# Performance work log

Hardware: AMD Instinct MI355X
Metric: run time of the kernel (lower is better)

## Reference

```python
import jax, jax.numpy as jnp
import numpy as np
from jax import lax

EPS = 1e-5
# PyTorch bicubic (a=-0.75), scale_factor=2, align_corners=False -> fixed 4-tap
# weights: even outputs use frac 0.75, odd outputs use frac 0.25.
W75 = jnp.array([-0.03515625, 0.26171875, 0.87890625, -0.10546875], dtype=jnp.float32)
W25 = W75[::-1]


def _up1d_2x(x, axis):
    x = jnp.moveaxis(x, axis, -1)
    n = x.shape[-1]
    pad = [(0, 0)] * (x.ndim - 1) + [(2, 2)]
    xp = jnp.pad(x, pad, mode='edge')  # replicate border like torch
    even = sum(W75[k] * xp[..., k:k + n] for k in range(4))
    odd = sum(W25[k] * xp[..., k + 1:k + 1 + n] for k in range(4))
    out = jnp.stack([even, odd], axis=-1).reshape(x.shape[:-1] + (2 * n,))
    return jnp.moveaxis(out, -1, axis)


def bicubic2x(x):  # [N,C,H,W] -> [N,C,2H,2W]
    return _up1d_2x(_up1d_2x(x, 2), 3)


def groupnorm1(x, w, b):  # GroupNorm(1, C): normalize over (C,H,W) per sample
    m = jnp.mean(x, axis=(1, 2, 3), keepdims=True)
    v = jnp.mean(jnp.square(x - m), axis=(1, 2, 3), keepdims=True)
    xh = (x - m) * lax.rsqrt(v + EPS)
    return xh * w[None, :, None, None] + b[None, :, None, None]


def conv3x3(x, w, b):
    y = lax.conv_general_dilated(x, w, (1, 1), ((1, 1), (1, 1)),
                                 dimension_numbers=('NCHW', 'OIHW', 'NCHW'))
    return y + b[None, :, None, None]


def setup_inputs() -> dict:
    key = jax.random.key(0)
    ks = jax.random.split(key, 24)
    B, C, H, W = 4, 256, 64, 64
    chans = [256, 64, 16, 4]  # embed_dim // 4**i
    inp = {'x': jax.random.normal(ks[0], (B, C, H, W), jnp.float32)}
    for j in range(4):
        s = 2 ** (j + 1)
        inp[f'em{j}'] = 0.1 * jax.random.normal(ks[1 + j], (B, chans[j], H * s, W * s), jnp.float32)
    for j, c in enumerate(chans):
        co = max(c // 4, 1)
        inp[f'gn_w{j}'] = 1.0 + 0.1 * jax.random.normal(ks[5 + 4 * j], (c,), jnp.float32)
        inp[f'gn_b{j}'] = 0.1 * jax.random.normal(ks[6 + 4 * j], (c,), jnp.float32)
        inp[f'cw{j}'] = jax.random.normal(ks[7 + 4 * j], (co, c, 3, 3), jnp.float32) / np.sqrt(9.0 * c)
        inp[f'cb{j}'] = 0.01 * jax.random.normal(ks[8 + 4 * j], (co,), jnp.float32)
    # per-sample (left, top, right, bottom) in the 64x64 grid; host-side ints
    # (in the original these come from get_bbox_from_mask on CPU)
    inp['bboxes'] = np.array([[8, 4, 56, 60], [0, 0, 48, 40],
                              [16, 8, 64, 56], [4, 12, 40, 64]], dtype=np.int32)
    return inp


def reference(x, em0, em1, em2, em3,
              gn_w0, gn_b0, cw0, cb0, gn_w1, gn_b1, cw1, cb1,
              gn_w2, gn_b2, cw2, cb2, gn_w3, gn_b3, cw3, cb3, bboxes):
    ems = [em0, em1, em2, em3]
    gws = [gn_w0, gn_w1, gn_w2, gn_w3]
    gbs = [gn_b0, gn_b1, gn_b2, gn_b3]
    cws = [cw0, cw1, cw2, cw3]
    cbs = [cb0, cb1, cb2, cb3]
    bb = np.asarray(bboxes)
    strides = [2, 4, 8, 16]
    B, _, H, W = x.shape
    mask = jnp.full((B, 1, H * 16, W * 16), -100.0, dtype=x.dtype)
    for i in range(B):  # per-sample ragged regions, as in the original eval loop
        l, t, r, b = (int(v) for v in bb[i])
        z = x[i:i + 1, :, t:b, l:r]
        for j in range(4):
            z = groupnorm1(z, gws[j], gbs[j])
            z = bicubic2x(z)
            s = strides[j]
            z = z + ems[j][i:i + 1, :, t * s:b * s, l * s:r * s]
            z = conv3x3(z, cws[j], cbs[j])
            if j < 3:
                z = jax.nn.silu(z)
        s = strides[-1]
        mask = mask.at[i:i + 1, :, t * s:b * s, l * s:r * s].set(z)
    return mask
```

## Files before the change

### kernel.cpp

```cpp
#include <hip/hip_runtime.h>

#define EPS 1e-5f

__global__ void fill_kernel(float* __restrict__ out, int n, float v) {
    int i = blockIdx.x * blockDim.x + threadIdx.x;
    if (i < n) out[i] = v;
}

__global__ void zero8_kernel(float* __restrict__ a) {
    if (threadIdx.x < 8) a[threadIdx.x] = 0.f;
}

__global__ void finalize_kernel(float* __restrict__ buf, long long batchStride,
                                int n, int ocShift, const float* __restrict__ bias,
                                int doSilu)
{
    int idx = blockIdx.x * blockDim.x + threadIdx.x;
    if (idx >= n) return;
    float* p = buf + (long long)blockIdx.y * batchStride;
    int oc = idx >> ocShift;
    float v = p[idx] + bias[oc];
    if (doSilu) v = v / (1.f + __expf(-v));
    p[idx] = v;
}

__global__ void gn_reduce_kernel(const float* __restrict__ in, long long inBatchStride,
                                 int inPitch, long long inPlane, int useOrig,
                                 int c, int shift, const int* __restrict__ bboxes,
                                 int batch0, float* __restrict__ accs)
{
    int batch = batch0 + blockIdx.z;
    const int* bb = bboxes + 4 * batch;
    int l = bb[0], t = bb[1], r = bb[2], btm = bb[3];
    int h = (btm - t) << shift;
    int w = (r   - l) << shift;
    int oy = useOrig ? t : 0;
    int ox = useOrig ? l : 0;
    const float* base = in + (long long)blockIdx.z * inBatchStride;

    float s = 0.f, s2 = 0.f;
    int stride = gridDim.x * blockDim.x;

    if (((w | ox | inPitch) & 3) == 0) {
        int w4 = w >> 2;
        int count4 = c * h * w4;
        for (int idx = blockIdx.x * blockDim.x + threadIdx.x; idx < count4; idx += stride) {
            int xw   = idx % w4;
            int rest = idx / w4;
            int y    = rest % h;
            int ch   = rest / h;
            const float4 v = *reinterpret_cast<const float4*>(
                base + (long long)ch * inPlane + (long long)(y + oy) * inPitch + (ox + 4 * xw));
            s  += (v.x + v.y) + (v.z + v.w);
            s2 += (v.x * v.x + v.y * v.y) + (v.z * v.z + v.w * v.w);
        }
    } else {
        int count = c * h * w;
        for (int idx = blockIdx.x * blockDim.x + threadIdx.x; idx < count; idx += stride) {
            int xw   = idx % w;
            int rest = idx / w;
            int y    = rest % h;
            int ch   = rest / h;
            float v = base[(long long)ch * inPlane + (long long)(y + oy) * inPitch + (xw + ox)];
            s  += v;
            s2 += v * v;
        }
    }

    for (int off = 32; off > 0; off >>= 1) {
        s  += __shfl_down(s, off);
        s2 += __shfl_down(s2, off);
    }
    __shared__ float red[2][4];
    int wid = threadIdx.x >> 6;
    if ((threadIdx.x & 63) == 0) { red[0][wid] = s; red[1][wid] = s2; }
    __syncthreads();
    if (threadIdx.x == 0) {
        float ts = (red[0][0] + red[0][1]) + (red[0][2] + red[0][3]);
        float t2 = (red[1][0] + red[1][1]) + (red[1][2] + red[1][3]);
        atomicAdd(&accs[2 * batch],     ts);
        atomicAdd(&accs[2 * batch + 1], t2);
    }
}

__global__ void normup_kernel(const float* __restrict__ in, long long inBatchStride,
                              int inPitch, long long inPlane, int useOrig,
                              const float* __restrict__ em, long long emBatchStride, int emPitch,
                              const float* __restrict__ gw, const float* __restrict__ gb,
                              const float* __restrict__ accs,
                              float* __restrict__ outB, long long outBatchStride, int outPitch,
                              int c, int shift, const int* __restrict__ bboxes,
                              int batch0, int tilesY)
{
    int batch = batch0 + blockIdx.z;
    const int* bb = bboxes + 4 * batch;
    int l = bb[0], t = bb[1], r = bb[2], btm = bb[3];
    int h = (btm - t) << shift;
    int w = (r   - l) << shift;
    int H2 = 2 * h, W2 = 2 * w;

    int ch = blockIdx.y / tilesY;
    int ty = blockIdx.y % tilesY;
    int y2 = ty * 16 + threadIdx.y;
    int x2 = blockIdx.x * 16 + threadIdx.x;
    if (y2 >= H2 || x2 >= W2) return;

    float count = (float)(c * h * w);
    float m  = accs[2 * batch] / count;
    float var = accs[2 * batch + 1] / count - m * m;
    float rs = rsqrtf(fmaxf(var, 0.f) + EPS);
    float alpha = rs * gw[ch];
    float beta  = gb[ch] - m * alpha;

    int oy = useOrig ? t : 0;
    int ox = useOrig ? l : 0;
    const float* base = in + (long long)blockIdx.z * inBatchStride + (long long)ch * inPlane;

    const float Wv[2][4] = {
        {-0.03515625f, 0.26171875f, 0.87890625f, -0.10546875f},
        {-0.10546875f, 0.87890625f, 0.26171875f, -0.03515625f}};

    int iy = y2 >> 1, py = y2 & 1;
    int ix = x2 >> 1, px = x2 & 1;
    int by = iy - 2 + py;
    int bx = ix - 2 + px;

    float acc = 0.f;
    #pragma unroll
    for (int a = 0; a < 4; a++) {
        int ry = by + a;
        ry = ry < 0 ? 0 : (ry > h - 1 ? h - 1 : ry);
        const float* rowp = base + (long long)(ry + oy) * inPitch + ox;
        float rsum = 0.f;
        #pragma unroll
        for (int q = 0; q < 4; q++) {
            int rx = bx + q;
            rx = rx < 0 ? 0 : (rx > w - 1 ? w - 1 : rx);
            rsum += Wv[px][q] * rowp[rx];
        }
        acc += Wv[py][a] * rsum;
    }

    float val = alpha * acc + beta;
    int S = 2 << shift;
    val += em[(long long)blockIdx.z * emBatchStride + (long long)ch * emPitch * emPitch
              + (long long)(t * S + y2) * emPitch + (l * S + x2)];

    outB[(long long)blockIdx.z * outBatchStride + (long long)ch * outPitch * outPitch
         + (long long)y2 * outPitch + x2] = val;
}

#define CICH 4

template<int COT>
__global__ void __launch_bounds__(256)
conv_reg_kernel(const float* __restrict__ inB, long long inBatchStride, int inPitch,
                const float* __restrict__ wts, const float* __restrict__ bias,
                int cin, int ciPer, int bShift, int doSilu,
                float* __restrict__ out, long long outBatchStride, int outPitch,
                int toMask, int doFinal, int shift, const int* __restrict__ bboxes,
                int batch0, int tilesY)
{
    int zb = blockIdx.z & ((1 << bShift) - 1);
    int sp = blockIdx.z >> bShift;
    int batch = batch0 + zb;
    const int* bb = bboxes + 4 * batch;
    int l = bb[0], t = bb[1], r = bb[2], btm = bb[3];
    int h = (btm - t) << shift;
    int w = (r   - l) << shift;
    int H2 = 2 * h, W2 = 2 * w;

    int og = blockIdx.y / tilesY;
    int ty = blockIdx.y % tilesY;
    int oc0 = og * COT;
    int y0 = ty * 32;
    int x0 = blockIdx.x * 32;
    if (y0 >= H2 || x0 >= W2) return;

    int ly = threadIdx.y, lx = threadIdx.x;
    int tid = ly * 16 + lx;
    int py0 = y0 + 2 * ly;
    int px0 = x0 + 2 * lx;

    __shared__ float tile[CICH][34][36];
    __shared__ __align__(16) float wsh[COT][CICH][12];

    const float* base = inB + (long long)zb * inBatchStride;
    long long plane = (long long)inPitch * inPitch;
    long long oplane = (long long)outPitch * outPitch;

    constexpr int TITEMS = CICH * 1156;
    constexpr int NIT    = (TITEMS + 255) / 256;
    constexpr int WITEMS = COT * CICH * 9;
    constexpr int NWIT   = (WITEMS + 255) / 256;

    float acc[COT][2][2];
    #pragma unroll
    for (int o = 0; o < COT; o++)
        #pragma unroll
        for (int rr = 0; rr < 2; rr++)
            #pragma unroll
            for (int ss = 0; ss < 2; ss++) acc[o][rr][ss] = 0.f;

    int ciStart = sp * ciPer;
    int ciEnd = ciStart + ciPer;
    for (int ci0 = ciStart; ci0 < ciEnd; ci0 += CICH) {
        float rbuf[NIT];
        #pragma unroll
        for (int it = 0; it < NIT; ++it) {
            int q = tid + it * 256;
            float v = 0.f;
            if (q < TITEMS) {
                int p   = q / 1156;
                int rem = q - p * 1156;
                int yy  = rem / 34;
                int xx  = rem - yy * 34;
                int gy = y0 - 1 + yy, gx = x0 - 1 + xx;
                if (gy >= 0 && gy < H2 && gx >= 0 && gx < W2)
                    v = base[(long long)(ci0 + p) * plane + (long long)gy * inPitch + gx];
            }
            rbuf[it] = v;
        }
        float wreg[NWIT];
        #pragma unroll
        for (int it = 0; it < NWIT; ++it) {
            int q = tid + it * 256;
            float v = 0.f;
            if (q < WITEMS) {
                int o   = q / (CICH * 9);
                int rem = q - o * (CICH * 9);
                int p   = rem / 9;
                int k   = rem - p * 9;
                v = wts[((long long)(oc0 + o) * cin + (ci0 + p)) * 9 + k];
            }
            wreg[it] = v;
        }
        #pragma unroll
        for (int it = 0; it < NIT; ++it) {
            int q = tid + it * 256;
            if (q < TITEMS) {
                int p   = q / 1156;
                int rem = q - p * 1156;
                int yy  = rem / 34;
                int xx  = rem - yy * 34;
                tile[p][yy][xx] = rbuf[it];
            }
        }
        #pragma unroll
        for (int it = 0; it < NWIT; ++it) {
            int q = tid + it * 256;
            if (q < WITEMS) {
                int o   = q / (CICH * 9);
                int rem = q - o * (CICH * 9);
                int p   = rem / 9;
                int k   = rem - p * 9;
                wsh[o][p][k] = wreg[it];
            }
        }
        __syncthreads();

        #pragma unroll
        for (int p = 0; p < CICH; p++) {
            float v[4][4];
            #pragma unroll
            for (int rr = 0; rr < 4; rr++) {
                const float2 a = *reinterpret_cast<const float2*>(&tile[p][2 * ly + rr][2 * lx]);
                const float2 b = *reinterpret_cast<const float2*>(&tile[p][2 * ly + rr][2 * lx + 2]);
                v[rr][0] = a.x; v[rr][1] = a.y; v[rr][2] = b.x; v[rr][3] = b.y;
            }
            #pragma unroll
            for (int o = 0; o < COT; o++) {
                const float4 wA = *reinterpret_cast<const float4*>(&wsh[o][p][0]);
                const float4 wB = *reinterpret_cast<const float4*>(&wsh[o][p][4]);
                const float  w8 = wsh[o][p][8];
                #pragma unroll
                for (int rr = 0; rr < 2; rr++) {
                    #pragma unroll
                    for (int ss = 0; ss < 2; ss++) {
                        acc[o][rr][ss] += wA.x * v[rr    ][ss] + wA.y * v[rr    ][ss + 1] + wA.z * v[rr    ][ss + 2]
                                        + wA.w * v[rr + 1][ss] + wB.x * v[rr + 1][ss + 1] + wB.y * v[rr + 1][ss + 2]
                                        + wB.z * v[rr + 2][ss] + wB.w * v[rr + 2][ss + 1] + w8   * v[rr + 2][ss + 2];
                    }
                }
            }
        }
        __syncthreads();
    }

    if (doFinal) {
        #pragma unroll
        for (int o = 0; o < COT; o++) {
            float b = bias[oc0 + o];
            #pragma unroll
            for (int rr = 0; rr < 2; rr++) {
                #pragma unroll
                for (int ss = 0; ss < 2; ss++) {
                    int oy2 = py0 + rr, ox2 = px0 + ss;
                    if (oy2 >= H2 || ox2 >= W2) continue;
                    float v = acc[o][rr][ss] + b;
                    if (doSilu) v = v / (1.f + __expf(-v));
                    if (toMask) {
                        int S = 2 << shift;
                        out[(long long)batch * 1024 * 1024 + (long long)(t * S + oy2) * 1024 + (l * S + ox2)] = v;
                    } else {
                        out[(long long)zb * outBatchStride + (long long)(oc0 + o) * oplane
                            + (long long)oy2 * outPitch + ox2] = v;
                    }
                }
            }
        }
    } else {
        #pragma unroll
        for (int o = 0; o < COT; o++) {
            #pragma unroll
            for (int rr = 0; rr < 2; rr++) {
                #pragma unroll
                for (int ss = 0; ss < 2; ss++) {
                    int oy2 = py0 + rr, ox2 = px0 + ss;
                    if (oy2 >= H2 || ox2 >= W2) continue;
                    atomicAdd(&out[(long long)zb * outBatchStride + (long long)(oc0 + o) * oplane
                                   + (long long)oy2 * outPitch + ox2], acc[o][rr][ss]);
                }
            }
        }
    }
}

static inline void launch_conv(int co, int tiles32, int nz, int S,
                               const float* inB, long long inBS, int inPitch,
                               const float* wts, const float* bias, int cin, int doSilu,
                               float* out, long long outBS, int outPitch,
                               int toMask, int shift, const int* bboxes, int batch0,
                               hipStream_t stream)
{
    dim3 blk(16, 16);
    int bShift = (nz == 4) ? 2 : 0;
    int ciPer = cin / S;
    int doFinal = (S == 1) ? 1 : 0;
    dim3 grid;
    if (co == 64)      grid = dim3(tiles32, tiles32 * 8, nz * S);
    else if (co == 16) grid = dim3(tiles32, tiles32 * 2, nz * S);
    else               grid = dim3(tiles32, tiles32,     nz * S);

    if (co == 64 || co == 16) {
        conv_reg_kernel<8><<<grid, blk, 0, stream>>>(
            inB, inBS, inPitch, wts, bias, cin, ciPer, bShift, doSilu,
            out, outBS, outPitch, toMask, doFinal, shift, bboxes, batch0, tiles32);
    } else if (co == 4) {
        conv_reg_kernel<4><<<grid, blk, 0, stream>>>(
            inB, inBS, inPitch, wts, bias, cin, ciPer, bShift, doSilu,
            out, outBS, outPitch, toMask, doFinal, shift, bboxes, batch0, tiles32);
    } else {
        conv_reg_kernel<1><<<grid, blk, 0, stream>>>(
            inB, inBS, inPitch, wts, bias, cin, ciPer, bShift, doSilu,
            out, outBS, outPitch, toMask, doFinal, shift, bboxes, batch0, tiles32);
    }
}

extern "C" void kernel_launch(void* const* d_in, const int* in_sizes, int n_in,
                              void* d_out, int out_size, void* d_ws, size_t ws_size,
                              hipStream_t stream)
{
    const float* x  = (const float*)d_in[0];
    const float* em[4];
    const float* gw[4];
    const float* gb[4];
    const float* cw[4];
    const float* cb[4];
    for (int j = 0; j < 4; j++) {
        em[j] = (const float*)d_in[1 + j];
        gw[j] = (const float*)d_in[5 + 4 * j];
        gb[j] = (const float*)d_in[6 + 4 * j];
        cw[j] = (const float*)d_in[7 + 4 * j];
        cb[j] = (const float*)d_in[8 + 4 * j];
    }
    const int* bboxes = (const int*)d_in[21];
    float* out = (float*)d_out;
    float* ws  = (float*)d_ws;

    const int chans[4] = {256, 64, 16, 4};
    const int couts[4] = {64, 16, 4, 1};
    const int splits[4] = {1, 1, 1, 1};

    const long long A_OFF  = 256;
    const long long A_SLOT = 1048576;
    const long long B_SLOT = 4194304;

    bool par = ws_size >= (size_t)(A_OFF + 4 * A_SLOT + 4 * B_SLOT) * 4;
    int nA = par ? 4 : 1;
    float* accs = ws;
    float* bufA = ws + A_OFF;
    float* bufB = ws + A_OFF + nA * A_SLOT;

    fill_kernel<<<(4194304 + 255) / 256, 256, 0, stream>>>(out, 4194304, -100.0f);

    if (par) {
        for (int j = 0; j < 4; j++) {
            int c = chans[j], co = couts[j], shift = j;
            int inPitch = 64 << j;
            long long inPlane = (long long)inPitch * inPitch;
            int upPitch = 128 << j;
            int tiles = upPitch / 16;
            int tiles32 = upPitch / 32;
            int E = 128 << j;
            long long emStride = (long long)c * E * E;
            int S = splits[j];

            const float* gin = (j == 0) ? x : bufA;
            long long ginStride = (j == 0) ? (long long)256 * 64 * 64 : A_SLOT;
            int useOrig = (j == 0) ? 1 : 0;

            zero8_kernel<<<1, 64, 0, stream>>>(accs);
            gn_reduce_kernel<<<dim3(512, 1, 4), 256, 0, stream>>>(
                gin, ginStride, inPitch, inPlane, useOrig, c, shift, bboxes, 0, accs);
            normup_kernel<<<dim3(tiles, tiles * c, 4), dim3(16, 16), 0, stream>>>(
                gin, ginStride, inPitch, inPlane, useOrig,
                em[j], emStride, E, gw[j], gb[j], accs,
                bufB, B_SLOT, upPitch, c, shift, bboxes, 0, tiles);
            if (S > 1) {
                fill_kernel<<<(int)((4 * A_SLOT + 255) / 256), 256, 0, stream>>>(
                    bufA, (int)(4 * A_SLOT), 0.f);
            }
            launch_conv(co, tiles32, 4, S,
                        bufB, B_SLOT, upPitch, cw[j], cb[j], c, (j < 3) ? 1 : 0,
                        (j < 3) ? bufA : out, (j < 3) ? A_SLOT : 0, upPitch,
                        (j == 3) ? 1 : 0, shift, bboxes, 0, stream);
            if (S > 1) {
                int ocShift = 2 * (7 + j);
                finalize_kernel<<<dim3(4096, 4), 256, 0, stream>>>(
                    bufA, A_SLOT, (int)A_SLOT, ocShift, cb[j], (j < 3) ? 1 : 0);
            }
        }
    } else {
        for (int i = 0; i < 4; i++) {
            for (int j = 0; j < 4; j++) {
                int c = chans[j], co = couts[j], shift = j;
                int inPitch = 64 << j;
                long long inPlane = (long long)inPitch * inPitch;
                int upPitch = 128 << j;
                int tiles = upPitch / 16;
                int tiles32 = upPitch / 32;
                int E = 128 << j;
                long long emStride = (long long)c * E * E;
                int S = splits[j];

                const float* gin = (j == 0) ? (x + (long long)i * 256 * 64 * 64) : bufA;
                int useOrig = (j == 0) ? 1 : 0;

                zero8_kernel<<<1, 64, 0, stream>>>(accs);
                gn_reduce_kernel<<<dim3(512, 1, 1), 256, 0, stream>>>(
                    gin, 0, inPitch, inPlane, useOrig, c, shift, bboxes, i, accs);
                normup_kernel<<<dim3(tiles, tiles * c, 1), dim3(16, 16), 0, stream>>>(
                    gin, 0, inPitch, inPlane, useOrig,
                    em[j] + (long long)i * emStride, 0, E, gw[j], gb[j], accs,
                    bufB, 0, upPitch, c, shift, bboxes, i, tiles);
                if (S > 1) {
                    fill_kernel<<<(int)((A_SLOT + 255) / 256), 256, 0, stream>>>(
                        bufA, (int)A_SLOT, 0.f);
                }
                launch_conv(co, tiles32, 1, S,
                            bufB, 0, upPitch, cw[j], cb[j], c, (j < 3) ? 1 : 0,
                            (j < 3) ? bufA : out, 0, upPitch,
                            (j == 3) ? 1 : 0, shift, bboxes, i, stream);
                if (S > 1) {
                    int ocShift = 2 * (7 + j);
                    finalize_kernel<<<dim3(4096, 1), 256, 0, stream>>>(
                        bufA, 0, (int)A_SLOT, ocShift, cb[j], (j < 3) ? 1 : 0);
                }
            }
        }
    }
}
```

Before: 1.429 ms.

## Double-buffer conv input/weight staging in registers and use 4 output channels per block

Restructures the channel-chunk loop of the register-tiled conv so the global loads for the next input/weight chunk are issued before computing the current chunk, using two register buffers. This overlaps global memory latency with FMA work. It also switches the co=64 and co=16 convs from 8 to 4 output channels per block, doubling the grid's y dimension. That raises parallelism but reloads each input tile twice as often and increases register pressure from the doubled staging buffers.

```diff
diff --git a/kernel.cpp b/kernel.cpp
--- a/kernel.cpp
+++ b/kernel.cpp
@@ -202,10 +202,7 @@
             #pragma unroll
             for (int ss = 0; ss < 2; ss++) acc[o][rr][ss] = 0.f;
 
-    int ciStart = sp * ciPer;
-    int ciEnd = ciStart + ciPer;
-    for (int ci0 = ciStart; ci0 < ciEnd; ci0 += CICH) {
-        float rbuf[NIT];
+    auto LOADA = [&](int ci0, float (&rb)[NIT], float (&wr)[NWIT]) {
         #pragma unroll
         for (int it = 0; it < NIT; ++it) {
             int q = tid + it * 256;
@@ -219,9 +216,8 @@
                 if (gy >= 0 && gy < H2 && gx >= 0 && gx < W2)
                     v = base[(long long)(ci0 + p) * plane + (long long)gy * inPitch + gx];
             }
-            rbuf[it] = v;
-        }
-        float wreg[NWIT];
+            rb[it] = v;
+        }
         #pragma unroll
         for (int it = 0; it < NWIT; ++it) {
             int q = tid + it * 256;
@@ -233,8 +229,11 @@
                 int k   = rem - p * 9;
                 v = wts[((long long)(oc0 + o) * cin + (ci0 + p)) * 9 + k];
             }
-            wreg[it] = v;
-        }
+            wr[it] = v;
+        }
+    };
+
+    auto WRITEB = [&](float (&rb)[NIT], float (&wr)[NWIT]) {
         #pragma unroll
         for (int it = 0; it < NIT; ++it) {
             int q = tid + it * 256;
@@ -243,7 +242,7 @@
                 int rem = q - p * 1156;
                 int yy  = rem / 34;
                 int xx  = rem - yy * 34;
-                tile[p][yy][xx] = rbuf[it];
+                tile[p][yy][xx] = rb[it];
             }
         }
         #pragma unroll
@@ -254,11 +253,12 @@
                 int rem = q - o * (CICH * 9);
                 int p   = rem / 9;
                 int k   = rem - p * 9;
-                wsh[o][p][k] = wreg[it];
-            }
-        }
-        __syncthreads();
-
+                wsh[o][p][k] = wr[it];
+            }
+        }
+    };
+
+    auto COMPUTE = [&]() {
         #pragma unroll
         for (int p = 0; p < CICH; p++) {
             float v[4][4];
@@ -284,7 +284,26 @@
                 }
             }
         }
+    };
+
+    int ciStart = sp * ciPer;
+    int ciEnd = ciStart + ciPer;
+    float rbA[NIT], wrA[NWIT], rbB[NIT], wrB[NWIT];
+    LOADA(ciStart, rbA, wrA);
+    for (int ci0 = ciStart; ci0 < ciEnd; ci0 += 2 * CICH) {
+        WRITEB(rbA, wrA);
         __syncthreads();
+        bool hasB = (ci0 + CICH) < ciEnd;
+        if (hasB) LOADA(ci0 + CICH, rbB, wrB);
+        COMPUTE();
+        __syncthreads();
+        if (hasB) {
+            WRITEB(rbB, wrB);
+            __syncthreads();
+            if (ci0 + 2 * CICH < ciEnd) LOADA(ci0 + 2 * CICH, rbA, wrA);
+            COMPUTE();
+            __syncthreads();
+        }
     }
 
     if (doFinal) {
@@ -338,15 +357,11 @@
     int ciPer = cin / S;
     int doFinal = (S == 1) ? 1 : 0;
     dim3 grid;
-    if (co == 64)      grid = dim3(tiles32, tiles32 * 8, nz * S);
-    else if (co == 16) grid = dim3(tiles32, tiles32 * 2, nz * S);
-    else               grid = dim3(tiles32, tiles32,     nz * S);
-
-    if (co == 64 || co == 16) {
-        conv_reg_kernel<8><<<grid, blk, 0, stream>>>(
-            inB, inBS, inPitch, wts, bias, cin, ciPer, bShift, doSilu,
-            out, outBS, outPitch, toMask, doFinal, shift, bboxes, batch0, tiles32);
-    } else if (co == 4) {
+    if (co == 64)      grid = dim3(tiles32, tiles32 * 16, nz * S);
+    else if (co == 16) grid = dim3(tiles32, tiles32 * 4,  nz * S);
+    else               grid = dim3(tiles32, tiles32,      nz * S);
+
+    if (co >= 4) {
         conv_reg_kernel<4><<<grid, blk, 0, stream>>>(
             inB, inBS, inPitch, wts, bias, cin, ciPer, bShift, doSilu,
             out, outBS, outPitch, toMask, doFinal, shift, bboxes, batch0, tiles32);
```

Measured after the change: 1.697 ms. 1.19x slower.
